# Kernel tuning notes

Measured on AMD Instinct MI355X. Metric: run time of the kernel, lower is better.

## Reference

```python
import jax, jax.numpy as jnp
import numpy as np

H, DH = 6, 64
D = H * DH
SQRT_DH = np.float32(np.sqrt(DH))


def _pool_norm(tok, ids):
    # masked mean pooling over tokens, then L2 normalize (Encoder.mean_pooling + normalize)
    mask = (ids > 0).astype(tok.dtype)[:, :, None]
    s = jnp.sum(tok * mask, axis=1) / jnp.clip(jnp.sum(mask, axis=1), 1e-9, None)
    return s / jnp.clip(jnp.linalg.norm(s, axis=1, keepdims=True), 1e-12, None)


def setup_inputs() -> dict:
    key = jax.random.key(0)
    ks = jax.random.split(key, 16)
    N_MSG, N_CON, L, E = 10000, 20000, 16, 128000
    s = 0.05
    eye = jnp.eye(DH, dtype=jnp.float32)
    inp = {}
    inp['tok_msg'] = jax.random.normal(ks[0], (N_MSG, L, D), jnp.float32)
    inp['tok_con'] = jax.random.normal(ks[1], (N_CON, L, D), jnp.float32)
    inp['ids_msg'] = jax.random.randint(ks[2], (N_MSG, L), 0, 100)
    inp['ids_con'] = jax.random.randint(ks[3], (N_CON, L), 0, 100)
    inp['src_cm'] = jax.random.randint(ks[4], (E,), 0, N_CON)
    inp['dst_cm'] = jax.random.randint(ks[5], (E,), 0, N_MSG)
    inp['src_mc'] = jax.random.randint(ks[6], (E,), 0, N_MSG)
    inp['dst_mc'] = jax.random.randint(ks[7], (E,), 0, N_CON)
    inp['lin_W'] = jax.random.normal(ks[8], (2, D, D), jnp.float32) * s
    inp['lin_b'] = jnp.zeros((2, D), jnp.float32)
    inp['kW'] = jax.random.normal(ks[9], (2, 2, D, D), jnp.float32) * s
    inp['kb'] = jnp.zeros((2, 2, D), jnp.float32)
    inp['qW'] = jax.random.normal(ks[10], (2, 2, D, D), jnp.float32) * s
    inp['qb'] = jnp.zeros((2, 2, D), jnp.float32)
    inp['vW'] = jax.random.normal(ks[11], (2, 2, D, D), jnp.float32) * s
    inp['vb'] = jnp.zeros((2, 2, D), jnp.float32)
    inp['aW'] = jax.random.normal(ks[12], (2, 2, D, D), jnp.float32) * s
    inp['ab'] = jnp.zeros((2, 2, D), jnp.float32)
    inp['a_rel'] = jax.random.normal(ks[13], (2, 2, H, DH, DH), jnp.float32) * s + eye
    inp['m_rel'] = jax.random.normal(ks[14], (2, 2, H, DH, DH), jnp.float32) * s + eye
    inp['p_rel'] = jnp.ones((2, 2, H), jnp.float32)
    inp['skip'] = jnp.ones((2, 2), jnp.float32)
    return inp


def _hgt_layer(xs, edges, kW, kb, qW, qb, vW, vb, aW, ab, a_rel, m_rel, p_rel, skip):
    # xs = [x_message, x_concept]; edges = ((src, dst) per edge type)
    k = [(xs[t] @ kW[t] + kb[t]).reshape(-1, H, DH) for t in (0, 1)]
    q = [(xs[t] @ qW[t] + qb[t]).reshape(-1, H, DH) for t in (0, 1)]
    v = [(xs[t] @ vW[t] + vb[t]).reshape(-1, H, DH) for t in (0, 1)]
    edge_meta = ((1, 0), (0, 1))  # edge type e -> (src_type, dst_type)
    agg = [None, None]
    for e, (s, d) in enumerate(edge_meta):
        si, di = edges[e]
        Nd = xs[d].shape[0]
        # relation-specific key/message transforms, per head: [E, H, DH]
        ke = jnp.einsum('ehd,hdf->ehf', k[s][si], a_rel[e])
        score = jnp.einsum('ehf,ehf->eh', q[d][di], ke) * p_rel[e] / SQRT_DH
        # softmax over incoming edges per destination node
        m = jax.ops.segment_max(score, di, num_segments=Nd)
        ex = jnp.exp(score - m[di])
        den = jax.ops.segment_sum(ex, di, num_segments=Nd)
        alpha = ex / den[di]
        msg = jnp.einsum('ehd,hdf->ehf', v[s][si], m_rel[e]) * alpha[:, :, None]
        agg[d] = jax.ops.segment_sum(msg, di, num_segments=Nd).reshape(Nd, D)
    out = []
    for t in (0, 1):
        o = jax.nn.gelu(agg[t], approximate=False) @ aW[t] + ab[t]
        a = jax.nn.sigmoid(skip[t])
        out.append(a * o + (1.0 - a) * xs[t])
    return out


def reference(tok_msg, tok_con, ids_msg, ids_con, src_cm, dst_cm, src_mc, dst_mc,
              lin_W, lin_b, kW, kb, qW, qb, vW, vb, aW, ab, a_rel, m_rel, p_rel, skip):
    x0 = jax.nn.relu(_pool_norm(tok_msg, ids_msg) @ lin_W[0] + lin_b[0])
    x1 = jax.nn.relu(_pool_norm(tok_con, ids_con) @ lin_W[1] + lin_b[1])
    edges = ((src_cm, dst_cm), (src_mc, dst_mc))
    xs = [x0, x1]
    for l in range(2):  # num_layers = 2 (hard-coded in MedicalEncoder)
        xs = _hgt_layer(xs, edges, kW[l], kb[l], qW[l], qb[l], vW[l], vb[l],
                        aW[l], ab[l], a_rel[l], m_rel[l], p_rel[l], skip[l])
    return xs[0]  # x_dict['message']
```

## Files before the change

### kernel.cpp

```cpp
#include <hip/hip_runtime.h>
#include <math.h>

#define H 6
#define DH 64
#define D 384
#define L 16
#define WSZ ((size_t)(D) * (D))
#define RSZ ((size_t)(H) * (DH) * (DH))

typedef __attribute__((ext_vector_type(8))) short short8;
typedef __attribute__((ext_vector_type(4))) float f32x4;
typedef unsigned int uint_;

__device__ __forceinline__ float bf2f(unsigned short u) {
  union { unsigned int i; float f; } x; x.i = ((unsigned int)u) << 16; return x.f;
}
__device__ __forceinline__ unsigned short f2bf(float f) {
  unsigned int x = __float_as_uint(f);
  x = x + 0x7fffu + ((x >> 16) & 1u);
  return (unsigned short)(x >> 16);
}
__device__ __forceinline__ float blo(unsigned int u) { return __uint_as_float(u << 16); }
__device__ __forceinline__ float bhi(unsigned int u) { return __uint_as_float(u & 0xffff0000u); }
__device__ __forceinline__ float geluf(float x) {
  return 0.5f * x * (1.0f + erff(x * 0.70710678118654752f));
}

__global__ void zero_int_kernel(int* p, long n) {
  long i = (long)blockIdx.x * blockDim.x + threadIdx.x;
  long stride = (long)gridDim.x * blockDim.x;
  for (; i < n; i += stride) p[i] = 0;
}

__global__ void pool_norm_kernel(const float* __restrict__ tokM, const int* __restrict__ idsM,
                                 unsigned short* __restrict__ outM, int NM,
                                 const float* __restrict__ tokC, const int* __restrict__ idsC,
                                 unsigned short* __restrict__ outC) {
  int n = blockIdx.x;
  const float* tok; const int* ids; unsigned short* out;
  if (n < NM) { tok = tokM; ids = idsM; out = outM; }
  else { n -= NM; tok = tokC; ids = idsC; out = outC; }
  int t = threadIdx.x;
  const float* tp = tok + (size_t)n * L * D;
  const int* ip = ids + (size_t)n * L;
  float s = 0.f;
  int cnt = 0;
#pragma unroll
  for (int l = 0; l < L; ++l) {
    int m = (ip[l] > 0);
    cnt += m;
    s += tp[(size_t)l * D + t] * (float)m;
  }
  float mean = s / fmaxf((float)cnt, 1e-9f);
  float v = mean * mean;
#pragma unroll
  for (int off = 32; off; off >>= 1) v += __shfl_down(v, off);
  __shared__ float part[D / 64];
  if ((t & 63) == 0) part[t >> 6] = v;
  __syncthreads();
  float tot = 0.f;
#pragma unroll
  for (int i = 0; i < D / 64; ++i) tot += part[i];
  float inv = 1.0f / fmaxf(sqrtf(tot), 1e-12f);
  out[(size_t)n * D + t] = f2bf(mean * inv);
}

__global__ void prepw_kernel(const float* __restrict__ lin_W, const float* __restrict__ kW,
                             const float* __restrict__ qW, const float* __restrict__ vW,
                             const float* __restrict__ aW, const float* __restrict__ a_rel,
                             const float* __restrict__ m_rel, unsigned short* __restrict__ wbuf) {
  int z = blockIdx.z;
  const float* src; const float* rel = nullptr; int type = 0;
  switch (z) {
    case 0: src = lin_W; break;
    case 1: src = lin_W + WSZ; break;
    case 2: src = kW; break;
    case 3: type = 1; src = qW; rel = a_rel; break;
    case 4: type = 2; src = vW; rel = m_rel + RSZ; break;
    case 5: src = kW + WSZ; break;
    case 6: type = 1; src = qW + WSZ; rel = a_rel + RSZ; break;
    case 7: type = 2; src = vW + WSZ; rel = m_rel; break;
    case 8: type = 1; src = qW + 2 * WSZ; rel = a_rel + 2 * RSZ; break;
    case 9: src = kW + 3 * WSZ; break;
    case 10: type = 2; src = vW + 3 * WSZ; rel = m_rel + 2 * RSZ; break;
    case 11: src = aW; break;
    case 12: src = aW + WSZ; break;
    default: src = aW + 2 * WSZ; break;
  }
  unsigned short* dst = wbuf + (size_t)z * WSZ;
  int tx = threadIdx.x, ty = threadIdx.y;
  int bx = blockIdx.x * 32;
  int by = blockIdx.y * 32;
  if (type == 0) {
    __shared__ float tile[32][33];
    tile[ty][tx] = src[(size_t)(bx + ty) * D + by + tx];
    __syncthreads();
    dst[(size_t)(by + ty) * D + bx + tx] = f2bf(tile[tx][ty]);
  } else if (type == 1) {
    int h = by >> 6, d0 = by & 63;
    __shared__ float Wt_[32][65], Rt[32][65];
#pragma unroll
    for (int half = 0; half < 2; ++half) {
      Wt_[ty][tx + half * 32] = src[(size_t)(bx + ty) * D + h * 64 + tx + half * 32];
      Rt[ty][tx + half * 32] = rel[(size_t)h * 4096 + (size_t)(d0 + ty) * 64 + tx + half * 32];
    }
    __syncthreads();
    float s = 0.f;
#pragma unroll 16
    for (int f = 0; f < 64; ++f) s += Wt_[tx][f] * Rt[ty][f];
    dst[(size_t)(by + ty) * D + bx + tx] = f2bf(s);
  } else {
    int h = by >> 6, f0 = by & 63;
    __shared__ float Wt_[32][65];
    __shared__ float Mt[64][33];
#pragma unroll
    for (int half = 0; half < 2; ++half) {
      Wt_[ty][tx + half * 32] = src[(size_t)(bx + ty) * D + h * 64 + tx + half * 32];
      Mt[ty * 2 + half][tx] = rel[(size_t)h * 4096 + (size_t)(ty * 2 + half) * 64 + f0 + tx];
    }
    __syncthreads();
    float s = 0.f;
#pragma unroll 16
    for (int d = 0; d < 64; ++d) s += Wt_[tx][d] * Mt[d][ty];
    dst[(size_t)(by + ty) * D + bx + tx] = f2bf(s);
  }
}

__global__ void prepb_kernel(const float* __restrict__ kb, const float* __restrict__ qb,
                             const float* __restrict__ vb, const float* __restrict__ a_rel,
                             const float* __restrict__ m_rel, float* __restrict__ bbuf) {
  int i = blockIdx.x * 256 + threadIdx.x;
  if (i >= 3456) return;
  int gemm, col;
  if (i < 1152) { gemm = 0; col = i; }
  else if (i < 2304) { gemm = 1; col = i - 1152; }
  else if (i < 2688) { gemm = 2; col = i - 2304; }
  else { gemm = 3; col = i - 2688; }
  int sec = col / D, j = col % D, h = j >> 6, r = j & 63;
  float out = 0.f;
  if (gemm == 0) {
    if (sec == 0) out = kb[j];
    else if (sec == 1) {
      const float* R = a_rel + (size_t)h * 4096 + (size_t)r * 64;
      float s = 0.f; for (int f = 0; f < 64; ++f) s += qb[h * 64 + f] * R[f]; out = s;
    } else {
      const float* Mm = m_rel + RSZ + (size_t)h * 4096;
      float s = 0.f; for (int d = 0; d < 64; ++d) s += vb[h * 64 + d] * Mm[d * 64 + r]; out = s;
    }
  } else if (gemm == 1) {
    if (sec == 0) out = kb[D + j];
    else if (sec == 1) {
      const float* R = a_rel + RSZ + (size_t)h * 4096 + (size_t)r * 64;
      float s = 0.f; for (int f = 0; f < 64; ++f) s += qb[D + h * 64 + f] * R[f]; out = s;
    } else {
      const float* Mm = m_rel + (size_t)h * 4096;
      float s = 0.f; for (int d = 0; d < 64; ++d) s += vb[D + h * 64 + d] * Mm[d * 64 + r]; out = s;
    }
  } else if (gemm == 2) {
    const float* R = a_rel + 2 * RSZ + (size_t)h * 4096 + (size_t)r * 64;
    float s = 0.f; for (int f = 0; f < 64; ++f) s += qb[2 * D + h * 64 + f] * R[f]; out = s;
  } else {
    if (sec == 0) out = kb[3 * D + j];
    else {
      const float* Mm = m_rel + 2 * RSZ + (size_t)h * 4096;
      float s = 0.f; for (int d = 0; d < 64; ++d) s += vb[3 * D + h * 64 + d] * Mm[d * 64 + r]; out = s;
    }
  }
  bbuf[i] = out;
}

__global__ void count2_kernel(const int* __restrict__ d0, const int* __restrict__ d1,
                              int* __restrict__ deg0, int* __restrict__ deg1, int E) {
  int e = blockIdx.x * blockDim.x + threadIdx.x;
  if (e < E) atomicAdd(&deg0[d0[e]], 1);
  else if (e < 2 * E) atomicAdd(&deg1[d1[e - E]], 1);
}

__global__ void scan2_kernel(const int* __restrict__ deg0, int* __restrict__ off0, int N0,
                             const int* __restrict__ deg1, int* __restrict__ off1, int N1) {
  const int* deg = blockIdx.x ? deg1 : deg0;
  int* off = blockIdx.x ? off1 : off0;
  int N = blockIdx.x ? N1 : N0;
  __shared__ int wsum[16];
  __shared__ int carrySh;
  int tid = threadIdx.x;
  int lane = tid & 63, wid = tid >> 6;
  if (tid == 0) carrySh = 0;
  __syncthreads();
  for (int base = 0; base < N; base += 1024) {
    int i = base + tid;
    int v = (i < N) ? deg[i] : 0;
    int s = v;
#pragma unroll
    for (int o = 1; o < 64; o <<= 1) {
      int t = __shfl_up(s, o);
      if (lane >= o) s += t;
    }
    if (lane == 63) wsum[wid] = s;
    __syncthreads();
    int wpre = 0;
    for (int j = 0; j < wid; ++j) wpre += wsum[j];
    int c = carrySh;
    if (i < N) off[i] = c + wpre + s - v;
    __syncthreads();
    if (tid == 1023) carrySh = c + wpre + s;
    __syncthreads();
  }
  if (tid == 0) off[N] = carrySh;
}

__global__ void scatter2_kernel(const int* __restrict__ d0, const int* __restrict__ s0,
                                const int* __restrict__ off0, int* __restrict__ cur0,
                                int* __restrict__ el0,
                                const int* __restrict__ d1, const int* __restrict__ s1,
                                const int* __restrict__ off1, int* __restrict__ cur1,
                                int* __restrict__ el1, int E) {
  int e = blockIdx.x * blockDim.x + threadIdx.x;
  if (e < E) {
    int d = d0[e];
    el0[off0[d] + atomicAdd(&cur0[d], 1)] = s0[e];
  } else if (e < 2 * E) {
    int ee = e - E;
    int d = d1[ee];
    el1[off1[d] + atomicAdd(&cur1[d], 1)] = s1[ee];
  }
}

struct AttnP {
  const unsigned short* kb;
  const unsigned short* tqb;
  const unsigned short* vmb;
  const int* off;
  const int* elist;
  const float* prel;
  unsigned short* aggb;
  int N, sk, st, sv, nb;
};

__global__ void attn_kernel(AttnP a0, AttnP a1) {
  bool first = (int)blockIdx.x < a0.nb;
  AttnP a = first ? a0 : a1;
  int bx = first ? (int)blockIdx.x : (int)blockIdx.x - a0.nb;
  int node = bx * 4 + (threadIdx.x >> 6);
  int lane = threadIdx.x & 63;
  if (node >= a.N) return;
  int e0 = a.off[node], e1 = a.off[node + 1];
  int half = lane >> 5;
  const uint_* tq32 = (const uint_*)(a.tqb + (size_t)node * a.st);
  float tq0[3], tq1[3], pr8[3], m[3], den[3], ac0[3], ac1[3];
#pragma unroll
  for (int j = 0; j < 3; ++j) {
    uint_ u = tq32[lane + 64 * j];
    tq0[j] = blo(u); tq1[j] = bhi(u);
    pr8[j] = a.prel[2 * j + half] * 0.125f;
    m[j] = -1e30f; den[j] = 0.f; ac0[j] = 0.f; ac1[j] = 0.f;
  }
  int i = e0;
  for (; i + 2 <= e1; i += 2) {
    int s0 = a.elist[i], s1 = a.elist[i + 1];
    const uint_* k0 = (const uint_*)(a.kb + (size_t)s0 * a.sk);
    const uint_* k1 = (const uint_*)(a.kb + (size_t)s1 * a.sk);
    const uint_* v0 = (const uint_*)(a.vmb + (size_t)s0 * a.sv);
    const uint_* v1 = (const uint_*)(a.vmb + (size_t)s1 * a.sv);
    float pa[3], pb[3]; uint_ va[3], vb[3];
#pragma unroll
    for (int j = 0; j < 3; ++j) {
      uint_ ka = k0[lane + 64 * j], kbu = k1[lane + 64 * j];
      va[j] = v0[lane + 64 * j]; vb[j] = v1[lane + 64 * j];
      pa[j] = blo(ka) * tq0[j] + bhi(ka) * tq1[j];
      pb[j] = blo(kbu) * tq0[j] + bhi(kbu) * tq1[j];
    }
#pragma unroll
    for (int o = 1; o <= 16; o <<= 1)
#pragma unroll
      for (int j = 0; j < 3; ++j) {
        pa[j] += __shfl_xor(pa[j], o);
        pb[j] += __shfl_xor(pb[j], o);
      }
#pragma unroll
    for (int j = 0; j < 3; ++j) {
      float x0 = pa[j] * pr8[j], x1 = pb[j] * pr8[j];
      float mn = fmaxf(m[j], fmaxf(x0, x1));
      float r = __expf(m[j] - mn);
      float p0 = __expf(x0 - mn);
      float p1 = __expf(x1 - mn);
      den[j] = den[j] * r + p0 + p1;
      ac0[j] = ac0[j] * r + p0 * blo(va[j]) + p1 * blo(vb[j]);
      ac1[j] = ac1[j] * r + p0 * bhi(va[j]) + p1 * bhi(vb[j]);
      m[j] = mn;
    }
  }
  if (i < e1) {
    int s0 = a.elist[i];
    const uint_* k0 = (const uint_*)(a.kb + (size_t)s0 * a.sk);
    const uint_* v0 = (const uint_*)(a.vmb + (size_t)s0 * a.sv);
    float pa[3]; uint_ va[3];
#pragma unroll
    for (int j = 0; j < 3; ++j) {
      uint_ ka = k0[lane + 64 * j];
      va[j] = v0[lane + 64 * j];
      pa[j] = blo(ka) * tq0[j] + bhi(ka) * tq1[j];
    }
#pragma unroll
    for (int o = 1; o <= 16; o <<= 1)
#pragma unroll
      for (int j = 0; j < 3; ++j) pa[j] += __shfl_xor(pa[j], o);
#pragma unroll
    for (int j = 0; j < 3; ++j) {
      float x0 = pa[j] * pr8[j];
      float mn = fmaxf(m[j], x0);
      float r = __expf(m[j] - mn);
      float p0 = __expf(x0 - mn);
      den[j] = den[j] * r + p0;
      ac0[j] = ac0[j] * r + p0 * blo(va[j]);
      ac1[j] = ac1[j] * r + p0 * bhi(va[j]);
      m[j] = mn;
    }
  }
  uint_* op32 = (uint_*)(a.aggb + (size_t)node * D);
#pragma unroll
  for (int j = 0; j < 3; ++j) {
    float o0 = (e1 > e0) ? ac0[j] / den[j] : 0.f;
    float o1 = (e1 > e0) ? ac1[j] / den[j] : 0.f;
    op32[lane + 64 * j] = (uint_)f2bf(geluf(o0)) | ((uint_)f2bf(geluf(o1)) << 16);
  }
}

struct GemmP {
  const unsigned short* A;
  const unsigned short* Wt;
  const float* bias;
  float* Cf;
  unsigned short* Cb;
  const float* xold;
  const float* skipPtr;
  int M, N, cpitch, relu;
};

__global__ __launch_bounds__(256) void gemm_bf16(GemmP q0, GemmP q1) {
  GemmP p = blockIdx.z ? q1 : q0;
  const int bm = blockIdx.x * 128, bn = blockIdx.y * 128;
  if (bm >= p.M || bn >= p.N) return;
  __shared__ __align__(16) unsigned short As[2][128 * 64];
  __shared__ __align__(16) unsigned short Bs[2][128 * 64];
  const int tid = threadIdx.x;
  const int w = tid >> 6, lane = tid & 63;

  auto stage = [&](int t, int buf) {
#pragma unroll
    for (int i = 0; i < 4; ++i) {
      int cid = (w * 4 + i) * 64 + lane;
      int row = cid >> 3;
      int cg = (cid & 7) ^ (row & 7);
      int grow = bm + row;
      if (grow >= p.M) grow = p.M - 1;
      const unsigned short* gp = p.A + (size_t)grow * D + t * 64 + cg * 8;
      __builtin_amdgcn_global_load_lds((const __attribute__((address_space(1))) void*)gp,
                                       (__attribute__((address_space(3))) void*)&As[buf][(w * 4 + i) * 512],
                                       16, 0, 0);
    }
#pragma unroll
    for (int i = 0; i < 4; ++i) {
      int cid = (w * 4 + i) * 64 + lane;
      int row = cid >> 3;
      int cg = (cid & 7) ^ (row & 7);
      const unsigned short* gp = p.Wt + (size_t)(bn + row) * D + t * 64 + cg * 8;
      __builtin_amdgcn_global_load_lds((const __attribute__((address_space(1))) void*)gp,
                                       (__attribute__((address_space(3))) void*)&Bs[buf][(w * 4 + i) * 512],
                                       16, 0, 0);
    }
  };

  stage(0, 0);
  __syncthreads();

  const int wr = w >> 1, wc = w & 1;
  const int la = lane & 15, hi = lane >> 4;
  f32x4 acc[4][4] = {};

  for (int t = 0; t < 6; ++t) {
    if (t < 5) stage(t + 1, (t + 1) & 1);
    const unsigned short* Ab = As[t & 1];
    const unsigned short* Bb = Bs[t & 1];
#pragma unroll
    for (int ks = 0; ks < 2; ++ks) {
      int c = ks * 4 + hi;
      short8 af[4], bfr[4];
#pragma unroll
      for (int mi = 0; mi < 4; ++mi) {
        int row = wr * 64 + mi * 16 + la;
        af[mi] = *(const short8*)&Ab[row * 64 + ((c ^ (row & 7)) * 8)];
      }
#pragma unroll
      for (int n = 0; n < 4; ++n) {
        int col = wc * 64 + n * 16 + la;
        bfr[n] = *(const short8*)&Bb[col * 64 + ((c ^ (col & 7)) * 8)];
      }
#pragma unroll
      for (int mi = 0; mi < 4; ++mi)
#pragma unroll
        for (int n = 0; n < 4; ++n)
          acc[mi][n] = __builtin_amdgcn_mfma_f32_16x16x32_bf16(af[mi], bfr[n], acc[mi][n], 0, 0, 0);
    }
    __syncthreads();
  }

  float sa = 0.f;
  if (p.xold) sa = 1.0f / (1.0f + __expf(-*p.skipPtr));
#pragma unroll
  for (int mi = 0; mi < 4; ++mi) {
#pragma unroll
    for (int n = 0; n < 4; ++n) {
#pragma unroll
      for (int r = 0; r < 4; ++r) {
        int row = bm + wr * 64 + mi * 16 + hi * 4 + r;
        int col = bn + wc * 64 + n * 16 + la;
        if (row >= p.M) continue;
        float v = acc[mi][n][r] + p.bias[col];
        if (p.relu) v = fmaxf(v, 0.f);
        if (p.xold) v = sa * v + (1.0f - sa) * p.xold[(size_t)row * D + col];
        if (p.Cf) p.Cf[(size_t)row * p.cpitch + col] = v;
        if (p.Cb) p.Cb[(size_t)row * p.cpitch + col] = f2bf(v);
      }
    }
  }
}

extern "C" void kernel_launch(void* const* d_in, const int* in_sizes, int n_in,
                              void* d_out, int out_size, void* d_ws, size_t ws_size,
                              hipStream_t stream) {
  const float* tok_msg = (const float*)d_in[0];
  const float* tok_con = (const float*)d_in[1];
  const int* ids_msg = (const int*)d_in[2];
  const int* ids_con = (const int*)d_in[3];
  const int* src_cm = (const int*)d_in[4];
  const int* dst_cm = (const int*)d_in[5];
  const int* src_mc = (const int*)d_in[6];
  const int* dst_mc = (const int*)d_in[7];
  const float* lin_W = (const float*)d_in[8];
  const float* lin_b = (const float*)d_in[9];
  const float* kW = (const float*)d_in[10];
  const float* kb = (const float*)d_in[11];
  const float* qW = (const float*)d_in[12];
  const float* qb = (const float*)d_in[13];
  const float* vW = (const float*)d_in[14];
  const float* vb = (const float*)d_in[15];
  const float* aW = (const float*)d_in[16];
  const float* ab = (const float*)d_in[17];
  const float* a_rel = (const float*)d_in[18];
  const float* m_rel = (const float*)d_in[19];
  const float* p_rel = (const float*)d_in[20];
  const float* skip = (const float*)d_in[21];

  const int NM = in_sizes[2] / L;
  const int NC = in_sizes[3] / L;
  const int E = in_sizes[4];

  char* wsb = (char*)d_ws;
  size_t woff = 0;
  auto alloc = [&](size_t bytes) {
    woff = (woff + 255) & ~(size_t)255;
    void* p = wsb + woff;
    woff += bytes;
    return p;
  };
  const size_t NMe = (size_t)NM * D, NCe = (size_t)NC * D;
  unsigned short* poolM = (unsigned short*)alloc(NMe * 2);
  unsigned short* poolC = (unsigned short*)alloc(NCe * 2);
  float* x0f = (float*)alloc(NMe * 4);
  float* x1f = (float*)alloc(NCe * 4);
  float* xn0f = (float*)alloc(NMe * 4);
  unsigned short* x0b = (unsigned short*)alloc(NMe * 2);
  unsigned short* x1b = (unsigned short*)alloc(NCe * 2);
  unsigned short* xn0b = (unsigned short*)alloc(NMe * 2);
  unsigned short* xn1b = (unsigned short*)alloc(NCe * 2);
  unsigned short* projM1 = (unsigned short*)alloc((size_t)NM * 1152 * 2);
  unsigned short* projC1 = (unsigned short*)alloc((size_t)NC * 1152 * 2);
  unsigned short* projM2 = (unsigned short*)alloc((size_t)NM * 384 * 2);
  unsigned short* projC2 = (unsigned short*)alloc((size_t)NC * 768 * 2);
  unsigned short* aggM = (unsigned short*)alloc(NMe * 2);
  unsigned short* aggC = (unsigned short*)alloc(NCe * 2);
  unsigned short* wbuf = (unsigned short*)alloc(14 * WSZ * 2);
  float* bbuf = (float*)alloc(3456 * 4);
  long nz = 2L * NM + 2L * NC;
  int* ibase = (int*)alloc((size_t)(nz + NM + 1 + NC + 1 + 2L * E) * 4);
  int* deg0 = ibase;
  int* cur0 = deg0 + NM;
  int* deg1 = cur0 + NM;
  int* cur1 = deg1 + NC;
  int* off0 = cur1 + NC;
  int* off1 = off0 + NM + 1;
  int* el0 = off1 + NC + 1;
  int* el1 = el0 + E;

  dim3 b256(256);
  const int mbM = (NM + 127) / 128, mbC = (NC + 127) / 128;
  const int mbMax = (mbM > mbC) ? mbM : mbC;

  prepw_kernel<<<dim3(12, 12, 14), dim3(32, 32), 0, stream>>>(lin_W, kW, qW, vW, aW, a_rel, m_rel, wbuf);
  prepb_kernel<<<14, b256, 0, stream>>>(kb, qb, vb, a_rel, m_rel, bbuf);

  zero_int_kernel<<<64, b256, 0, stream>>>(ibase, nz);
  int eg2 = (2 * E + 255) / 256;
  count2_kernel<<<eg2, b256, 0, stream>>>(dst_cm, dst_mc, deg0, deg1, E);
  scan2_kernel<<<2, 1024, 0, stream>>>(deg0, off0, NM, deg1, off1, NC);
  scatter2_kernel<<<eg2, b256, 0, stream>>>(dst_cm, src_cm, off0, cur0, el0,
                                            dst_mc, src_mc, off1, cur1, el1, E);

  pool_norm_kernel<<<NM + NC, D, 0, stream>>>(tok_msg, ids_msg, poolM, NM, tok_con, ids_con, poolC);

  {
    GemmP p0 = {poolM, wbuf, lin_b, x0f, x0b, nullptr, nullptr, NM, D, D, 1};
    GemmP p1 = {poolC, wbuf + WSZ, lin_b + D, x1f, x1b, nullptr, nullptr, NC, D, D, 1};
    gemm_bf16<<<dim3(mbMax, 3, 2), b256, 0, stream>>>(p0, p1);
  }
  {
    GemmP p0 = {x0b, wbuf + 2 * WSZ, bbuf, nullptr, projM1, nullptr, nullptr, NM, 1152, 1152, 0};
    GemmP p1 = {x1b, wbuf + 5 * WSZ, bbuf + 1152, nullptr, projC1, nullptr, nullptr, NC, 1152, 1152, 0};
    gemm_bf16<<<dim3(mbMax, 9, 2), b256, 0, stream>>>(p0, p1);
  }
  {
    AttnP a0 = {projC1, projM1 + 384, projC1 + 768, off0, el0, p_rel, aggM, NM, 1152, 1152, 1152, (NM + 3) / 4};
    AttnP a1 = {projM1, projC1 + 384, projM1 + 768, off1, el1, p_rel + H, aggC, NC, 1152, 1152, 1152, (NC + 3) / 4};
    attn_kernel<<<(NM + 3) / 4 + (NC + 3) / 4, b256, 0, stream>>>(a0, a1);
  }
  {
    GemmP p0 = {aggM, wbuf + 11 * WSZ, ab, xn0f, xn0b, x0f, skip + 0, NM, D, D, 0};
    GemmP p1 = {aggC, wbuf + 12 * WSZ, ab + D, nullptr, xn1b, x1f, skip + 1, NC, D, D, 0};
    gemm_bf16<<<dim3(mbMax, 3, 2), b256, 0, stream>>>(p0, p1);
  }
  {
    GemmP p0 = {xn0b, wbuf + 8 * WSZ, bbuf + 2304, nullptr, projM2, nullptr, nullptr, NM, 384, 384, 0};
    GemmP p1 = {xn1b, wbuf + 9 * WSZ, bbuf + 2688, nullptr, projC2, nullptr, nullptr, NC, 768, 768, 0};
    gemm_bf16<<<dim3(mbMax, 6, 2), b256, 0, stream>>>(p0, p1);
  }
  {
    AttnP a0 = {projC2, projM2, projC2 + 384, off0, el0, p_rel + 2 * H, aggM, NM, 768, 384, 768, (NM + 3) / 4};
    AttnP a1 = a0;
    attn_kernel<<<(NM + 3) / 4, b256, 0, stream>>>(a0, a1);
  }
  {
    GemmP p0 = {aggM, wbuf + 13 * WSZ, ab + 2 * D, (float*)d_out, nullptr, xn0f, skip + 2, NM, D, D, 0};
    GemmP p1 = p0;
    gemm_bf16<<<dim3(mbM, 3, 1), b256, 0, stream>>>(p0, p1);
  }
}
```

Baseline: 658.7 us.

## Vectorize pooling loads, fold p_rel scaling into weights, unroll attention edges by four

```diff
diff --git a/kernel.cpp b/kernel.cpp
--- a/kernel.cpp
+++ b/kernel.cpp
@@ -41,46 +41,69 @@
   if (n < NM) { tok = tokM; ids = idsM; out = outM; }
   else { n -= NM; tok = tokC; ids = idsC; out = outC; }
   int t = threadIdx.x;
-  const float* tp = tok + (size_t)n * L * D;
+  int rg = t / 96, c4 = t % 96;
+  const float4* tp = (const float4*)(tok + (size_t)n * L * D);
   const int* ip = ids + (size_t)n * L;
-  float s = 0.f;
   int cnt = 0;
 #pragma unroll
-  for (int l = 0; l < L; ++l) {
-    int m = (ip[l] > 0);
-    cnt += m;
-    s += tp[(size_t)l * D + t] * (float)m;
-  }
-  float mean = s / fmaxf((float)cnt, 1e-9f);
-  float v = mean * mean;
-#pragma unroll
-  for (int off = 32; off; off >>= 1) v += __shfl_down(v, off);
-  __shared__ float part[D / 64];
-  if ((t & 63) == 0) part[t >> 6] = v;
+  for (int l = 0; l < L; ++l) cnt += (ip[l] > 0);
+  float4 s = {0.f, 0.f, 0.f, 0.f};
+#pragma unroll
+  for (int li = 0; li < 4; ++li) {
+    int l = rg + li * 4;
+    if (ip[l] > 0) {
+      float4 v = tp[l * 96 + c4];
+      s.x += v.x; s.y += v.y; s.z += v.z; s.w += v.w;
+    }
+  }
+  __shared__ float4 part[4][96];
+  part[rg][c4] = s;
+  __syncthreads();
+  float4 m4 = {0.f, 0.f, 0.f, 0.f};
+  float dot = 0.f;
+  float inv_cnt = 1.0f / fmaxf((float)cnt, 1e-9f);
+  if (t < 96) {
+    float4 a = part[0][t], b = part[1][t], c = part[2][t], d2 = part[3][t];
+    m4.x = (a.x + b.x + c.x + d2.x) * inv_cnt;
+    m4.y = (a.y + b.y + c.y + d2.y) * inv_cnt;
+    m4.z = (a.z + b.z + c.z + d2.z) * inv_cnt;
+    m4.w = (a.w + b.w + c.w + d2.w) * inv_cnt;
+    dot = m4.x * m4.x + m4.y * m4.y + m4.z * m4.z + m4.w * m4.w;
+  }
+#pragma unroll
+  for (int o = 32; o; o >>= 1) dot += __shfl_down(dot, o);
+  __shared__ float wpart[6];
+  if ((t & 63) == 0) wpart[t >> 6] = dot;
   __syncthreads();
   float tot = 0.f;
 #pragma unroll
-  for (int i = 0; i < D / 64; ++i) tot += part[i];
+  for (int i = 0; i < 6; ++i) tot += wpart[i];
   float inv = 1.0f / fmaxf(sqrtf(tot), 1e-12f);
-  out[(size_t)n * D + t] = f2bf(mean * inv);
+  if (t < 96) {
+    uint2 o;
+    o.x = (uint_)f2bf(m4.x * inv) | ((uint_)f2bf(m4.y * inv) << 16);
+    o.y = (uint_)f2bf(m4.z * inv) | ((uint_)f2bf(m4.w * inv) << 16);
+    ((uint2*)(out + (size_t)n * D))[t] = o;
+  }
 }
 
 __global__ void prepw_kernel(const float* __restrict__ lin_W, const float* __restrict__ kW,
                              const float* __restrict__ qW, const float* __restrict__ vW,
                              const float* __restrict__ aW, const float* __restrict__ a_rel,
-                             const float* __restrict__ m_rel, unsigned short* __restrict__ wbuf) {
+                             const float* __restrict__ m_rel, const float* __restrict__ p_rel,
+                             unsigned short* __restrict__ wbuf) {
   int z = blockIdx.z;
-  const float* src; const float* rel = nullptr; int type = 0;
+  const float* src; const float* rel = nullptr; const float* prl = nullptr; int type = 0;
   switch (z) {
     case 0: src = lin_W; break;
     case 1: src = lin_W + WSZ; break;
     case 2: src = kW; break;
-    case 3: type = 1; src = qW; rel = a_rel; break;
+    case 3: type = 1; src = qW; rel = a_rel; prl = p_rel; break;
     case 4: type = 2; src = vW; rel = m_rel + RSZ; break;
     case 5: src = kW + WSZ; break;
-    case 6: type = 1; src = qW + WSZ; rel = a_rel + RSZ; break;
+    case 6: type = 1; src = qW + WSZ; rel = a_rel + RSZ; prl = p_rel + H; break;
     case 7: type = 2; src = vW + WSZ; rel = m_rel; break;
-    case 8: type = 1; src = qW + 2 * WSZ; rel = a_rel + 2 * RSZ; break;
+    case 8: type = 1; src = qW + 2 * WSZ; rel = a_rel + 2 * RSZ; prl = p_rel + 2 * H; break;
     case 9: src = kW + 3 * WSZ; break;
     case 10: type = 2; src = vW + 3 * WSZ; rel = m_rel + 2 * RSZ; break;
     case 11: src = aW; break;
@@ -98,6 +121,7 @@
     dst[(size_t)(by + ty) * D + bx + tx] = f2bf(tile[tx][ty]);
   } else if (type == 1) {
     int h = by >> 6, d0 = by & 63;
+    float sc = prl[h] * 0.125f;
     __shared__ float Wt_[32][65], Rt[32][65];
 #pragma unroll
     for (int half = 0; half < 2; ++half) {
@@ -108,7 +132,7 @@
     float s = 0.f;
 #pragma unroll 16
     for (int f = 0; f < 64; ++f) s += Wt_[tx][f] * Rt[ty][f];
-    dst[(size_t)(by + ty) * D + bx + tx] = f2bf(s);
+    dst[(size_t)(by + ty) * D + bx + tx] = f2bf(s * sc);
   } else {
     int h = by >> 6, f0 = by & 63;
     __shared__ float Wt_[32][65];
@@ -128,7 +152,8 @@
 
 __global__ void prepb_kernel(const float* __restrict__ kb, const float* __restrict__ qb,
                              const float* __restrict__ vb, const float* __restrict__ a_rel,
-                             const float* __restrict__ m_rel, float* __restrict__ bbuf) {
+                             const float* __restrict__ m_rel, const float* __restrict__ p_rel,
+                             float* __restrict__ bbuf) {
   int i = blockIdx.x * 256 + threadIdx.x;
   if (i >= 3456) return;
   int gemm, col;
@@ -142,7 +167,8 @@
     if (sec == 0) out = kb[j];
     else if (sec == 1) {
       const float* R = a_rel + (size_t)h * 4096 + (size_t)r * 64;
-      float s = 0.f; for (int f = 0; f < 64; ++f) s += qb[h * 64 + f] * R[f]; out = s;
+      float s = 0.f; for (int f = 0; f < 64; ++f) s += qb[h * 64 + f] * R[f];
+      out = s * p_rel[h] * 0.125f;
     } else {
       const float* Mm = m_rel + RSZ + (size_t)h * 4096;
       float s = 0.f; for (int d = 0; d < 64; ++d) s += vb[h * 64 + d] * Mm[d * 64 + r]; out = s;
@@ -151,14 +177,16 @@
     if (sec == 0) out = kb[D + j];
     else if (sec == 1) {
       const float* R = a_rel + RSZ + (size_t)h * 4096 + (size_t)r * 64;
-      float s = 0.f; for (int f = 0; f < 64; ++f) s += qb[D + h * 64 + f] * R[f]; out = s;
+      float s = 0.f; for (int f = 0; f < 64; ++f) s += qb[D + h * 64 + f] * R[f];
+      out = s * p_rel[H + h] * 0.125f;
     } else {
       const float* Mm = m_rel + (size_t)h * 4096;
       float s = 0.f; for (int d = 0; d < 64; ++d) s += vb[D + h * 64 + d] * Mm[d * 64 + r]; out = s;
     }
   } else if (gemm == 2) {
     const float* R = a_rel + 2 * RSZ + (size_t)h * 4096 + (size_t)r * 64;
-    float s = 0.f; for (int f = 0; f < 64; ++f) s += qb[2 * D + h * 64 + f] * R[f]; out = s;
+    float s = 0.f; for (int f = 0; f < 64; ++f) s += qb[2 * D + h * 64 + f] * R[f];
+    out = s * p_rel[2 * H + h] * 0.125f;
   } else {
     if (sec == 0) out = kb[3 * D + j];
     else {
@@ -232,7 +260,6 @@
   const unsigned short* vmb;
   const int* off;
   const int* elist;
-  const float* prel;
   unsigned short* aggb;
   int N, sk, st, sv, nb;
 };
@@ -245,52 +272,58 @@
   int lane = threadIdx.x & 63;
   if (node >= a.N) return;
   int e0 = a.off[node], e1 = a.off[node + 1];
-  int half = lane >> 5;
   const uint_* tq32 = (const uint_*)(a.tqb + (size_t)node * a.st);
-  float tq0[3], tq1[3], pr8[3], m[3], den[3], ac0[3], ac1[3];
+  float tq0[3], tq1[3], m[3], den[3], ac0[3], ac1[3];
 #pragma unroll
   for (int j = 0; j < 3; ++j) {
     uint_ u = tq32[lane + 64 * j];
     tq0[j] = blo(u); tq1[j] = bhi(u);
-    pr8[j] = a.prel[2 * j + half] * 0.125f;
     m[j] = -1e30f; den[j] = 0.f; ac0[j] = 0.f; ac1[j] = 0.f;
   }
   int i = e0;
-  for (; i + 2 <= e1; i += 2) {
-    int s0 = a.elist[i], s1 = a.elist[i + 1];
-    const uint_* k0 = (const uint_*)(a.kb + (size_t)s0 * a.sk);
-    const uint_* k1 = (const uint_*)(a.kb + (size_t)s1 * a.sk);
-    const uint_* v0 = (const uint_*)(a.vmb + (size_t)s0 * a.sv);
-    const uint_* v1 = (const uint_*)(a.vmb + (size_t)s1 * a.sv);
-    float pa[3], pb[3]; uint_ va[3], vb[3];
+  for (; i + 4 <= e1; i += 4) {
+    int s[4];
+#pragma unroll
+    for (int u = 0; u < 4; ++u) s[u] = a.elist[i + u];
+    uint_ kk[4][3], vv[4][3];
+#pragma unroll
+    for (int u = 0; u < 4; ++u) {
+      const uint_* kp = (const uint_*)(a.kb + (size_t)s[u] * a.sk);
+      const uint_* vp = (const uint_*)(a.vmb + (size_t)s[u] * a.sv);
+#pragma unroll
+      for (int j = 0; j < 3; ++j) { kk[u][j] = kp[lane + 64 * j]; vv[u][j] = vp[lane + 64 * j]; }
+    }
+    float p[4][3];
+#pragma unroll
+    for (int u = 0; u < 4; ++u)
+#pragma unroll
+      for (int j = 0; j < 3; ++j)
+        p[u][j] = blo(kk[u][j]) * tq0[j] + bhi(kk[u][j]) * tq1[j];
+#pragma unroll
+    for (int o = 1; o <= 16; o <<= 1)
+#pragma unroll
+      for (int u = 0; u < 4; ++u)
+#pragma unroll
+        for (int j = 0; j < 3; ++j) p[u][j] += __shfl_xor(p[u][j], o);
 #pragma unroll
     for (int j = 0; j < 3; ++j) {
-      uint_ ka = k0[lane + 64 * j], kbu = k1[lane + 64 * j];
-      va[j] = v0[lane + 64 * j]; vb[j] = v1[lane + 64 * j];
-      pa[j] = blo(ka) * tq0[j] + bhi(ka) * tq1[j];
-      pb[j] = blo(kbu) * tq0[j] + bhi(kbu) * tq1[j];
-    }
-#pragma unroll
-    for (int o = 1; o <= 16; o <<= 1)
-#pragma unroll
-      for (int j = 0; j < 3; ++j) {
-        pa[j] += __shfl_xor(pa[j], o);
-        pb[j] += __shfl_xor(pb[j], o);
+      float mx = fmaxf(fmaxf(p[0][j], p[1][j]), fmaxf(p[2][j], p[3][j]));
+      float mn = fmaxf(m[j], mx);
+      float r = __expf(m[j] - mn);
+      float e_[4];
+#pragma unroll
+      for (int u = 0; u < 4; ++u) e_[u] = __expf(p[u][j] - mn);
+      den[j] = den[j] * r + e_[0] + e_[1] + e_[2] + e_[3];
+      float a0_ = ac0[j] * r, a1_ = ac1[j] * r;
+#pragma unroll
+      for (int u = 0; u < 4; ++u) {
+        a0_ += e_[u] * blo(vv[u][j]);
+        a1_ += e_[u] * bhi(vv[u][j]);
       }
-#pragma unroll
-    for (int j = 0; j < 3; ++j) {
-      float x0 = pa[j] * pr8[j], x1 = pb[j] * pr8[j];
-      float mn = fmaxf(m[j], fmaxf(x0, x1));
-      float r = __expf(m[j] - mn);
-      float p0 = __expf(x0 - mn);
-      float p1 = __expf(x1 - mn);
-      den[j] = den[j] * r + p0 + p1;
-      ac0[j] = ac0[j] * r + p0 * blo(va[j]) + p1 * blo(vb[j]);
-      ac1[j] = ac1[j] * r + p0 * bhi(va[j]) + p1 * bhi(vb[j]);
-      m[j] = mn;
-    }
-  }
-  if (i < e1) {
+      ac0[j] = a0_; ac1[j] = a1_; m[j] = mn;
+    }
+  }
+  for (; i < e1; ++i) {
     int s0 = a.elist[i];
     const uint_* k0 = (const uint_*)(a.kb + (size_t)s0 * a.sk);
     const uint_* v0 = (const uint_*)(a.vmb + (size_t)s0 * a.sv);
@@ -307,10 +340,9 @@
       for (int j = 0; j < 3; ++j) pa[j] += __shfl_xor(pa[j], o);
 #pragma unroll
     for (int j = 0; j < 3; ++j) {
-      float x0 = pa[j] * pr8[j];
-      float mn = fmaxf(m[j], x0);
+      float mn = fmaxf(m[j], pa[j]);
       float r = __expf(m[j] - mn);
-      float p0 = __expf(x0 - mn);
+      float p0 = __expf(pa[j] - mn);
       den[j] = den[j] * r + p0;
       ac0[j] = ac0[j] * r + p0 * blo(va[j]);
       ac1[j] = ac1[j] * r + p0 * bhi(va[j]);
@@ -497,8 +529,8 @@
   const int mbM = (NM + 127) / 128, mbC = (NC + 127) / 128;
   const int mbMax = (mbM > mbC) ? mbM : mbC;
 
-  prepw_kernel<<<dim3(12, 12, 14), dim3(32, 32), 0, stream>>>(lin_W, kW, qW, vW, aW, a_rel, m_rel, wbuf);
-  prepb_kernel<<<14, b256, 0, stream>>>(kb, qb, vb, a_rel, m_rel, bbuf);
+  prepw_kernel<<<dim3(12, 12, 14), dim3(32, 32), 0, stream>>>(lin_W, kW, qW, vW, aW, a_rel, m_rel, p_rel, wbuf);
+  prepb_kernel<<<14, b256, 0, stream>>>(kb, qb, vb, a_rel, m_rel, p_rel, bbuf);
 
   zero_int_kernel<<<64, b256, 0, stream>>>(ibase, nz);
   int eg2 = (2 * E + 255) / 256;
@@ -520,8 +552,8 @@
     gemm_bf16<<<dim3(mbMax, 9, 2), b256, 0, stream>>>(p0, p1);
   }
   {
-    AttnP a0 = {projC1, projM1 + 384, projC1 + 768, off0, el0, p_rel, aggM, NM, 1152, 1152, 1152, (NM + 3) / 4};
-    AttnP a1 = {projM1, projC1 + 384, projM1 + 768, off1, el1, p_rel + H, aggC, NC, 1152, 1152, 1152, (NC + 3) / 4};
+    AttnP a0 = {projC1, projM1 + 384, projC1 + 768, off0, el0, aggM, NM, 1152, 1152, 1152, (NM + 3) / 4};
+    AttnP a1 = {projM1, projC1 + 384, projM1 + 768, off1, el1, aggC, NC, 1152, 1152, 1152, (NC + 3) / 4};
     attn_kernel<<<(NM + 3) / 4 + (NC + 3) / 4, b256, 0, stream>>>(a0, a1);
   }
   {
@@ -535,7 +567,7 @@
     gemm_bf16<<<dim3(mbMax, 6, 2), b256, 0, stream>>>(p0, p1);
   }
   {
-    AttnP a0 = {projC2, projM2, projC2 + 384, off0, el0, p_rel + 2 * H, aggM, NM, 768, 384, 768, (NM + 3) / 4};
+    AttnP a0 = {projC2, projM2, projC2 + 384, off0, el0, aggM, NM, 768, 384, 768, (NM + 3) / 4};
     AttnP a1 = a0;
     attn_kernel<<<(NM + 3) / 4, b256, 0, stream>>>(a0, a1);
   }
```

New measurement: 689.6 us, median of 2. 4.7% more time.
